# Performance work log

Measured on AMD Instinct MI355X. Metric: run time of the kernel, lower is better.

The kernel has to match this reference:

```python
import jax, jax.numpy as jnp
import numpy as np

N, H, W = 4, 96, 96
C, G, K = 128, 8, 3
GC = C // G          # group channels = 16
P = K * K            # sampling points per group = 9
PAD = K // 2
OFS = 1.0            # offset_scale
HID = 4 * C          # mlp hidden
EPS = 1e-5           # torch nn.LayerNorm default eps


def _ln(x, g, b):
    m = jnp.mean(x, -1, keepdims=True)
    v = jnp.mean((x - m) ** 2, -1, keepdims=True)
    return (x - m) * jax.lax.rsqrt(v + EPS) * g + b


def _dcnv3_core(x, offset, mask):
    # x: (n,H,W,C) channels-last, offset: (n,H,W,G*P*2), mask: (n,H,W,G,P) softmaxed.
    # Faithful port of dcnv3_core_pytorch (stride=1, dilation=1, zero-pad grid_sample,
    # align_corners=False -> pixel = loc*size - 0.5).
    n = x.shape[0]
    xp = jnp.pad(x, ((0, 0), (PAD, PAD), (PAD, PAD), (0, 0)))
    Hin, Win = H + 2 * PAD, W + 2 * PAD
    L = H * W
    base = (K - 1) // 2 + 0.5
    ref_x = (base + jnp.arange(W, dtype=x.dtype)) / Win  # normalized by padded size
    ref_y = (base + jnp.arange(H, dtype=x.dtype)) / Hin
    k = jnp.arange(K, dtype=x.dtype) - (K - 1) // 2
    dx = jnp.repeat(k, K) / Win  # torch meshgrid('ij'): kernel-x varies slowest
    dy = jnp.tile(k, K) / Hin
    off = offset.reshape(n, H, W, G, P, 2)
    # absolute sampling pixel coords (grid_sample align_corners=False)
    px = (ref_x[None, None, :, None, None] + dx * OFS + off[..., 0] * OFS / Win) * Win - 0.5
    py = (ref_y[None, :, None, None, None] + dy * OFS + off[..., 1] * OFS / Hin) * Hin - 0.5
    # layout (n,G,L,P)
    px = px.transpose(0, 3, 1, 2, 4).reshape(n, G, L, P)
    py = py.transpose(0, 3, 1, 2, 4).reshape(n, G, L, P)
    mk = mask.transpose(0, 3, 1, 2, 4).reshape(n, G, L, P)
    xg = xp.reshape(n, Hin * Win, G, GC).transpose(0, 2, 1, 3)
    x0 = jnp.floor(px); y0 = jnp.floor(py)
    fx = px - x0; fy = py - y0
    x0 = x0.astype(jnp.int32); y0 = y0.astype(jnp.int32)
    x1 = x0 + 1; y1 = y0 + 1
    out = jnp.zeros((n, G, L, GC), x.dtype)
    for yi, xi, w in ((y0, x0, (1 - fy) * (1 - fx)), (y0, x1, (1 - fy) * fx),
                      (y1, x0, fy * (1 - fx)), (y1, x1, fy * fx)):
        valid = (yi >= 0) & (yi < Hin) & (xi >= 0) & (xi < Win)
        idx = jnp.clip(yi, 0, Hin - 1) * Win + jnp.clip(xi, 0, Win - 1)
        v = jnp.take_along_axis(xg, idx.reshape(n, G, L * P, 1), axis=2)
        v = v.reshape(n, G, L, P, GC)
        out = out + jnp.einsum('nglp,nglpc->nglc', jnp.where(valid, w, 0.0) * mk, v)
    return out.transpose(0, 2, 1, 3).reshape(n, H, W, C)


def _dcn(x, w_in, b_in, dw_k, dw_b, dwg, dwb, w_off, b_off, w_msk, b_msk, w_out, b_out):
    n = x.shape[0]
    xproj = x @ w_in + b_in
    x1 = jax.lax.conv_general_dilated(
        x, dw_k, (1, 1), 'SAME',
        dimension_numbers=('NHWC', 'HWIO', 'NHWC'),
        feature_group_count=C) + dw_b
    x1 = jax.nn.gelu(_ln(x1, dwg, dwb), approximate=False)
    offset = x1 @ w_off + b_off
    mask = jax.nn.softmax((x1 @ w_msk + b_msk).reshape(n, H, W, G, P), axis=-1)
    y = _dcnv3_core(xproj, offset, mask)
    return y @ w_out + b_out


def setup_inputs() -> dict:
    key = jax.random.key(0)
    ks = jax.random.split(key, 10)
    rn = lambda k, s, sc: jax.random.normal(k, s, jnp.float32) * sc
    return {
        'x': rn(ks[0], (N, H, W, C), 1.0),
        'ln1g': jnp.ones((C,), jnp.float32), 'ln1b': jnp.zeros((C,), jnp.float32),
        'w_in': rn(ks[1], (C, C), 0.02), 'b_in': jnp.zeros((C,), jnp.float32),
        'dw_k': rn(ks[2], (K, K, 1, C), 0.1), 'dw_b': jnp.zeros((C,), jnp.float32),
        'dwg': jnp.ones((C,), jnp.float32), 'dwb': jnp.zeros((C,), jnp.float32),
        'w_off': rn(ks[3], (C, G * P * 2), 0.01), 'b_off': rn(ks[4], (G * P * 2,), 0.1),
        'w_msk': rn(ks[5], (C, G * P), 0.02), 'b_msk': jnp.zeros((G * P,), jnp.float32),
        'w_out': rn(ks[6], (C, C), 0.02), 'b_out': jnp.zeros((C,), jnp.float32),
        'ln2g': jnp.ones((C,), jnp.float32), 'ln2b': jnp.zeros((C,), jnp.float32),
        'w1': rn(ks[7], (C, HID), 0.02), 'b1': jnp.zeros((HID,), jnp.float32),
        'w2': rn(ks[8], (HID, C), 0.02), 'b2': jnp.zeros((C,), jnp.float32),
    }


def reference(x, ln1g, ln1b, w_in, b_in, dw_k, dw_b, dwg, dwb, w_off, b_off,
              w_msk, b_msk, w_out, b_out, ln2g, ln2b, w1, b1, w2, b2):
    # pre-norm InternImage block: x = x + dcn(LN1(x)); x = x + mlp(LN2(x))
    x = x + _dcn(_ln(x, ln1g, ln1b), w_in, b_in, dw_k, dw_b, dwg, dwb,
                 w_off, b_off, w_msk, b_msk, w_out, b_out)
    h = _ln(x, ln2g, ln2b)
    h = jax.nn.gelu(h @ w1 + b1, approximate=False) @ w2 + b2
    return x + h
```

## Files before the change

### kernel.cpp

```cpp
#include <hip/hip_runtime.h>
#include <hip/hip_bf16.h>
#include <math.h>

using bf16 = __hip_bfloat16;
using bf162 = __hip_bfloat162;

typedef __bf16 bf16x8 __attribute__((ext_vector_type(8)));
typedef float floatx4 __attribute__((ext_vector_type(4)));

constexpr int NB = 4, HH = 96, WW = 96, CC = 128, GG = 8, PP = 9;
constexpr int HW = HH * WW;
constexpr int NPIX = NB * HW;

__device__ __forceinline__ float ld1(const float* p) { return *p; }
__device__ __forceinline__ float ld1(const bf16* p)  { return __bfloat162float(*p); }
__device__ __forceinline__ void st1(float* p, float v) { *p = v; }
__device__ __forceinline__ void st1(bf16* p, float v)  { *p = __float2bfloat16(v); }
__device__ __forceinline__ float b2f(bf16 v) { return __bfloat162float(v); }
__device__ __forceinline__ bf16 f2b(float v) { return __float2bfloat16(v); }
__device__ __forceinline__ float gelu_exact(float v) {
    return 0.5f * v * (1.0f + erff(v * 0.7071067811865475f));
}
__device__ __forceinline__ floatx4 MFMA(bf16x8 a, bf16x8 b, floatx4 c) {
    return __builtin_amdgcn_mfma_f32_16x16x32_bf16(a, b, c, 0, 0, 0);
}

struct PrepArgs {
    const float* src[6];
    bf16* dst[6];
    int K[6], N[6];
    int cum[7];
    const float* b_off; const float* b_msk; float* b_om;
};

__global__ __launch_bounds__(256) void prep_weights(PrepArgs pa, int total)
{
    int t = blockIdx.x * 256 + threadIdx.x;
    if (t >= total) return;
    if (t >= pa.cum[6]) {
        int e = t - pa.cum[6];
        pa.b_om[e] = (e < 144) ? pa.b_off[e] : pa.b_msk[e - 144];
        return;
    }
    int i = 0;
    #pragma unroll
    for (int j = 0; j < 5; ++j) if (t >= pa.cum[j + 1]) i = j + 1;
    int e = t - pa.cum[i];
    int Ki = pa.K[i], Ni = pa.N[i];
    int n = e / Ki, k = e - n * Ki;
    pa.dst[i][e] = f2b(pa.src[i][(size_t)k * Ni + n]);
}

template<typename TI, typename TO>
__global__ __launch_bounds__(256) void ln_kernel(
    const TI* __restrict__ X, const float* __restrict__ g,
    const float* __restrict__ b, TO* __restrict__ out)
{
    int wave = (blockIdx.x * 256 + threadIdx.x) >> 6;
    int lane = threadIdx.x & 63;
    if (wave >= NPIX) return;
    const TI* xp = X + (size_t)wave * 128 + 2 * lane;
    float v0 = ld1(xp), v1 = ld1(xp + 1);
    float s = v0 + v1, q = v0 * v0 + v1 * v1;
    #pragma unroll
    for (int o = 32; o; o >>= 1) { s += __shfl_xor(s, o); q += __shfl_xor(q, o); }
    float mean = s * (1.0f / 128.0f);
    float rstd = rsqrtf(q * (1.0f / 128.0f) - mean * mean + 1e-5f);
    float g0 = g[2 * lane], g1 = g[2 * lane + 1];
    float b0 = b[2 * lane], b1 = b[2 * lane + 1];
    TO* op = out + (size_t)wave * 128 + 2 * lane;
    st1(op,     (v0 - mean) * rstd * g0 + b0);
    st1(op + 1, (v1 - mean) * rstd * g1 + b1);
}

__global__ __launch_bounds__(256) void dwconv_ln_gelu_kernel(
    const bf16* __restrict__ xln, const float* __restrict__ dwk,
    const float* __restrict__ dwb, const float* __restrict__ gam,
    const float* __restrict__ bet, bf16* __restrict__ out)
{
    int wave = (blockIdx.x * 256 + threadIdx.x) >> 6;
    int lane = threadIdx.x & 63;
    if (wave >= NPIX) return;
    int n = wave / HW; int rem = wave % HW;
    int y = rem / WW;  int x = rem % WW;
    const bf162* xp = (const bf162*)xln;
    float a0 = 0.f, a1 = 0.f;
    #pragma unroll
    for (int ky = 0; ky < 3; ++ky) {
        int yy = y + ky - 1;
        if (yy < 0 || yy >= HH) continue;
        #pragma unroll
        for (int kx = 0; kx < 3; ++kx) {
            int xx = x + kx - 1;
            if (xx < 0 || xx >= WW) continue;
            bf162 v = xp[((size_t)(n * HH + yy) * WW + xx) * 64 + lane];
            const float* w = dwk + (ky * 3 + kx) * CC + 2 * lane;
            a0 = fmaf(b2f(v.x), w[0], a0);
            a1 = fmaf(b2f(v.y), w[1], a1);
        }
    }
    a0 += dwb[2 * lane]; a1 += dwb[2 * lane + 1];
    float s = a0 + a1, q = a0 * a0 + a1 * a1;
    #pragma unroll
    for (int o = 32; o; o >>= 1) { s += __shfl_xor(s, o); q += __shfl_xor(q, o); }
    float mean = s * (1.0f / 128.0f);
    float rstd = rsqrtf(q * (1.0f / 128.0f) - mean * mean + 1e-5f);
    float h0 = gelu_exact((a0 - mean) * rstd * gam[2 * lane]     + bet[2 * lane]);
    float h1 = gelu_exact((a1 - mean) * rstd * gam[2 * lane + 1] + bet[2 * lane + 1]);
    bf162 o2; o2.x = f2b(h0); o2.y = f2b(h1);
    ((bf162*)out)[(size_t)wave * 64 + lane] = o2;
}

__global__ __launch_bounds__(256) void gemm_mfma_kernel(
    const bf16* __restrict__ A, const bf16* __restrict__ Wt,
    const float* __restrict__ bias, bf16* __restrict__ Out, int M, int Nn)
{
    __shared__ __align__(16) __bf16 As[64][136];
    __shared__ __align__(16) __bf16 Bs[64][136];
    int tid = threadIdx.x;
    int wv = tid >> 6, lane = tid & 63;
    int bm = blockIdx.y * 64, bn = blockIdx.x * 64;
    int mI = lane & 15, q = lane >> 4;

    #pragma unroll
    for (int i = 0; i < 4; ++i) {
        int s = tid + 256 * i;
        int row = s >> 4, ko = (s & 15) * 8;
        *reinterpret_cast<uint4*>(&As[row][ko]) =
            *reinterpret_cast<const uint4*>(A + (size_t)(bm + row) * 128 + ko);
        int ng = bn + row;
        uint4 bv = make_uint4(0, 0, 0, 0);
        if (ng < Nn) bv = *reinterpret_cast<const uint4*>(Wt + (size_t)ng * 128 + ko);
        *reinterpret_cast<uint4*>(&Bs[row][ko]) = bv;
    }
    __syncthreads();

    floatx4 acc[4] = {};
    #pragma unroll
    for (int ks = 0; ks < 4; ++ks) {
        int k = ks * 32 + q * 8;
        bf16x8 a = *reinterpret_cast<const bf16x8*>(&As[wv * 16 + mI][k]);
        #pragma unroll
        for (int t = 0; t < 4; ++t) {
            bf16x8 b = *reinterpret_cast<const bf16x8*>(&Bs[t * 16 + mI][k]);
            acc[t] = MFMA(a, b, acc[t]);
        }
    }
    int row0 = bm + wv * 16 + q * 4;
    #pragma unroll
    for (int t = 0; t < 4; ++t) {
        int col = bn + t * 16 + mI;
        if (col >= Nn) continue;
        float bs = bias[col];
        #pragma unroll
        for (int r = 0; r < 4; ++r)
            st1(Out + (size_t)(row0 + r) * Nn + col, acc[t][r] + bs);
    }
}

constexpr int SOMR = 228;
__global__ __launch_bounds__(256) void dcn_fused_kernel(
    const bf16* __restrict__ xproj, const bf16* __restrict__ x1,
    const bf16* __restrict__ w_omT, const float* __restrict__ b_om,
    bf16* __restrict__ out)
{
    __shared__ __align__(16) __bf16 sX1[16][136];
    __shared__ __align__(16) __bf16 sOmr[16][SOMR];
    __shared__ int4   sOff[4][72];
    __shared__ float4 sW[4][72];
    int tid = threadIdx.x, wv = tid >> 6, lane = tid & 63;
    int mI = lane & 15, q = lane >> 4;
    int bp = blockIdx.x * 16;

    {
        int row = tid >> 4, ko = (tid & 15) * 8;
        *reinterpret_cast<uint4*>(&sX1[row][ko]) =
            *reinterpret_cast<const uint4*>(x1 + (size_t)(bp + row) * 128 + ko);
    }
    __syncthreads();

    {
        bf16x8 a[4];
        #pragma unroll
        for (int ks = 0; ks < 4; ++ks)
            a[ks] = *reinterpret_cast<const bf16x8*>(&sX1[mI][ks * 32 + q * 8]);
        for (int t = wv; t < 14; t += 4) {
            int ng = t * 16 + mI;
            floatx4 acc = {};
            #pragma unroll
            for (int ks = 0; ks < 4; ++ks) {
                bf16x8 b = {};
                if (ng < 216)
                    b = *reinterpret_cast<const bf16x8*>(
                        w_omT + (size_t)ng * 128 + ks * 32 + q * 8);
                acc = MFMA(a[ks], b, acc);
            }
            float bs = (ng < 216) ? b_om[ng] : 0.f;
            #pragma unroll
            for (int r = 0; r < 4; ++r)
                sOmr[q * 4 + r][ng] = *(__bf16*)&(const bf16&)f2b(acc[r] + bs);
        }
    }
    __syncthreads();

    for (int pp = 0; pp < 4; ++pp) {
        int pr = wv * 4 + pp;
        int pix = bp + pr;
        int n = pix / HW; int rem = pix % HW;
        int iy = rem / WW; int ix = rem % WW;

        for (int e = lane; e < 72; e += 64) {
            int g = e / 9, p = e - 9 * g;
            float mx = -1e30f;
            #pragma unroll
            for (int i = 0; i < 9; ++i)
                mx = fmaxf(mx, b2f(*(const bf16*)&sOmr[pr][144 + g * 9 + i]));
            float ssum = 0.f;
            #pragma unroll
            for (int i = 0; i < 9; ++i)
                ssum += __expf(b2f(*(const bf16*)&sOmr[pr][144 + g * 9 + i]) - mx);
            float mw = __expf(b2f(*(const bf16*)&sOmr[pr][144 + e]) - mx) / ssum;

            float ox = b2f(*(const bf16*)&sOmr[pr][g * 18 + 2 * p]);
            float oy = b2f(*(const bf16*)&sOmr[pr][g * 18 + 2 * p + 1]);
            int kx = p / 3 - 1, ky = p % 3 - 1;
            float px = (float)(ix + kx) + ox;
            float py = (float)(iy + ky) + oy;
            float fx0 = floorf(px), fy0 = floorf(py);
            int x0 = (int)fx0, y0 = (int)fy0;
            float fx = px - fx0, fy = py - fy0;
            bool vx0 = (x0 >= 0) & (x0 < WW), vx1 = (x0 + 1 >= 0) & (x0 + 1 < WW);
            bool vy0 = (y0 >= 0) & (y0 < HH), vy1 = (y0 + 1 >= 0) & (y0 + 1 < HH);
            float w00 = (1.f - fy) * (1.f - fx) * mw * (vy0 && vx0 ? 1.f : 0.f);
            float w01 = (1.f - fy) * fx         * mw * (vy0 && vx1 ? 1.f : 0.f);
            float w10 = fy * (1.f - fx)         * mw * (vy1 && vx0 ? 1.f : 0.f);
            float w11 = fy * fx                 * mw * (vy1 && vx1 ? 1.f : 0.f);
            int x0c = min(max(x0, 0), WW - 1), x1c = min(max(x0 + 1, 0), WW - 1);
            int y0c = min(max(y0, 0), HH - 1), y1c = min(max(y0 + 1, 0), HH - 1);
            sOff[wv][e] = make_int4((y0c * WW + x0c) * CC, (y0c * WW + x1c) * CC,
                                    (y1c * WW + x0c) * CC, (y1c * WW + x1c) * CC);
            sW[wv][e] = make_float4(w00, w01, w10, w11);
        }

        const bf16* xb = xproj + (size_t)n * HW * CC + 2 * lane;
        int gbase = (lane >> 3) * 9;
        float a0 = 0.f, a1 = 0.f;
        #pragma unroll
        for (int p = 0; p < 9; ++p) {
            int4 o = sOff[wv][gbase + p];
            float4 w = sW[wv][gbase + p];
            bf162 v00 = *(const bf162*)(xb + o.x);
            bf162 v01 = *(const bf162*)(xb + o.y);
            bf162 v10 = *(const bf162*)(xb + o.z);
            bf162 v11 = *(const bf162*)(xb + o.w);
            a0 += w.x * b2f(v00.x) + w.y * b2f(v01.x) + w.z * b2f(v10.x) + w.w * b2f(v11.x);
            a1 += w.x * b2f(v00.y) + w.y * b2f(v01.y) + w.z * b2f(v10.y) + w.w * b2f(v11.y);
        }
        bf162 o2; o2.x = f2b(a0); o2.y = f2b(a1);
        ((bf162*)out)[(size_t)pix * 64 + lane] = o2;
    }
}

__global__ __launch_bounds__(256, 3) void fused_tail_kernel(
    const bf16* __restrict__ ycore, const float* __restrict__ x,
    const bf16* __restrict__ w_outT, const float* __restrict__ b_out,
    const float* __restrict__ ln2g, const float* __restrict__ ln2b,
    const bf16* __restrict__ w1T, const float* __restrict__ b1,
    const bf16* __restrict__ w2T, const float* __restrict__ b2,
    float* __restrict__ out)
{
    __shared__ __align__(16) bf16 sA[64 * 136];
    __shared__ __align__(16) bf16 sXres[64 * 136];
    __shared__ __align__(16) bf16 sH2[64 * 136];
    int tid = threadIdx.x, wv = tid >> 6, lane = tid & 63;
    int mI = lane & 15, q = lane >> 4;
    int bm = blockIdx.x * 64;

    bf16x8 bw0[4][2];
    #pragma unroll
    for (int ks = 0; ks < 4; ++ks)
        #pragma unroll
        for (int ct = 0; ct < 2; ++ct)
            bw0[ks][ct] = *reinterpret_cast<const bf16x8*>(
                w_outT + (size_t)(wv * 32 + ct * 16 + mI) * 128 + ks * 32 + q * 8);

    #pragma unroll
    for (int i = 0; i < 4; ++i) {
        int s = tid + 256 * i;
        int row = s >> 4, ko = (s & 15) * 8;
        *reinterpret_cast<uint4*>(&sA[row * 136 + ko]) =
            *reinterpret_cast<const uint4*>(ycore + (size_t)(bm + row) * 128 + ko);
    }
    __syncthreads();

    floatx4 acc0[4][2] = {};
    #pragma unroll
    for (int ks = 0; ks < 4; ++ks) {
        int k = ks * 32 + q * 8;
        bf16x8 a[4];
        #pragma unroll
        for (int rt = 0; rt < 4; ++rt)
            a[rt] = *reinterpret_cast<const bf16x8*>(&sA[(rt * 16 + mI) * 136 + k]);
        #pragma unroll
        for (int ct = 0; ct < 2; ++ct)
            #pragma unroll
            for (int rt = 0; rt < 4; ++rt)
                acc0[rt][ct] = MFMA(a[rt], bw0[ks][ct], acc0[rt][ct]);
    }
    #pragma unroll
    for (int rt = 0; rt < 4; ++rt)
        #pragma unroll
        for (int ct = 0; ct < 2; ++ct) {
            int col = wv * 32 + ct * 16 + mI;
            float bs = b_out[col];
            #pragma unroll
            for (int r = 0; r < 4; ++r) {
                int row = rt * 16 + q * 4 + r;
                float v = acc0[rt][ct][r] + bs + x[(size_t)(bm + row) * 128 + col];
                sXres[row * 136 + col] = f2b(v);
            }
        }
    __syncthreads();

    {
        int row = tid >> 2, part = tid & 3;
        float s = 0.f, sq = 0.f;
        float vals[32];
        #pragma unroll
        for (int j = 0; j < 4; ++j) {
            bf16x8 v = *reinterpret_cast<const bf16x8*>(&sXres[row * 136 + part * 32 + j * 8]);
            #pragma unroll
            for (int e = 0; e < 8; ++e) {
                float f = (float)v[e];
                vals[j * 8 + e] = f; s += f; sq += f * f;
            }
        }
        s  += __shfl_xor(s, 1);  s += __shfl_xor(s, 2);
        sq += __shfl_xor(sq, 1); sq += __shfl_xor(sq, 2);
        float mean = s * (1.0f / 128.0f);
        float rstd = rsqrtf(sq * (1.0f / 128.0f) - mean * mean + 1e-5f);
        #pragma unroll
        for (int j = 0; j < 4; ++j) {
            bf16x8 o;
            #pragma unroll
            for (int e = 0; e < 8; ++e) {
                int ch = part * 32 + j * 8 + e;
                bf16 t = f2b((vals[j * 8 + e] - mean) * rstd * ln2g[ch] + ln2b[ch]);
                o[e] = *reinterpret_cast<__bf16*>(&t);
            }
            *reinterpret_cast<bf16x8*>(&sH2[row * 136 + part * 32 + j * 8]) = o;
        }
    }
    __syncthreads();

    floatx4 acc2[4][2] = {};
    #pragma unroll 1
    for (int ph = 0; ph < 4; ++ph) {
        bf16x8 bw1[4][2];
        #pragma unroll
        for (int ks = 0; ks < 4; ++ks)
            #pragma unroll
            for (int ct = 0; ct < 2; ++ct)
                bw1[ks][ct] = *reinterpret_cast<const bf16x8*>(
                    w1T + (size_t)(ph * 128 + wv * 32 + ct * 16 + mI) * 128 + ks * 32 + q * 8);
        floatx4 acc1[4][2] = {};
        #pragma unroll
        for (int ks = 0; ks < 4; ++ks) {
            int k = ks * 32 + q * 8;
            bf16x8 a[4];
            #pragma unroll
            for (int rt = 0; rt < 4; ++rt)
                a[rt] = *reinterpret_cast<const bf16x8*>(&sH2[(rt * 16 + mI) * 136 + k]);
            #pragma unroll
            for (int ct = 0; ct < 2; ++ct)
                #pragma unroll
                for (int rt = 0; rt < 4; ++rt)
                    acc1[rt][ct] = MFMA(a[rt], bw1[ks][ct], acc1[rt][ct]);
        }
        __syncthreads();
        bf16x8 bw2[4][2];
        #pragma unroll
        for (int ks = 0; ks < 4; ++ks)
            #pragma unroll
            for (int ct = 0; ct < 2; ++ct)
                bw2[ks][ct] = *reinterpret_cast<const bf16x8*>(
                    w2T + (size_t)(wv * 32 + ct * 16 + mI) * 512 + ph * 128 + ks * 32 + q * 8);
        #pragma unroll
        for (int rt = 0; rt < 4; ++rt)
            #pragma unroll
            for (int ct = 0; ct < 2; ++ct) {
                int lcol = wv * 32 + ct * 16 + mI;
                float bs = b1[ph * 128 + lcol];
                #pragma unroll
                for (int r = 0; r < 4; ++r) {
                    int row = rt * 16 + q * 4 + r;
                    sA[row * 136 + lcol] = f2b(gelu_exact(acc1[rt][ct][r] + bs));
                }
            }
        __syncthreads();
        #pragma unroll
        for (int ks = 0; ks < 4; ++ks) {
            int k = ks * 32 + q * 8;
            bf16x8 a[4];
            #pragma unroll
            for (int rt = 0; rt < 4; ++rt)
                a[rt] = *reinterpret_cast<const bf16x8*>(&sA[(rt * 16 + mI) * 136 + k]);
            #pragma unroll
            for (int ct = 0; ct < 2; ++ct)
                #pragma unroll
                for (int rt = 0; rt < 4; ++rt)
                    acc2[rt][ct] = MFMA(a[rt], bw2[ks][ct], acc2[rt][ct]);
        }
    }
    #pragma unroll
    for (int rt = 0; rt < 4; ++rt)
        #pragma unroll
        for (int ct = 0; ct < 2; ++ct) {
            int col = wv * 32 + ct * 16 + mI;
            float bs = b2[col];
            #pragma unroll
            for (int r = 0; r < 4; ++r) {
                int row = rt * 16 + q * 4 + r;
                out[(size_t)(bm + row) * 128 + col] =
                    acc2[rt][ct][r] + bs + b2f(sXres[row * 136 + col]);
            }
        }
}

extern "C" void kernel_launch(void* const* d_in, const int* in_sizes, int n_in,
                              void* d_out, int out_size, void* d_ws, size_t ws_size,
                              hipStream_t stream)
{
    const float* x     = (const float*)d_in[0];
    const float* ln1g  = (const float*)d_in[1];
    const float* ln1b  = (const float*)d_in[2];
    const float* w_in  = (const float*)d_in[3];
    const float* b_in  = (const float*)d_in[4];
    const float* dw_k  = (const float*)d_in[5];
    const float* dw_b  = (const float*)d_in[6];
    const float* dwg   = (const float*)d_in[7];
    const float* dwb   = (const float*)d_in[8];
    const float* w_off = (const float*)d_in[9];
    const float* b_off = (const float*)d_in[10];
    const float* w_msk = (const float*)d_in[11];
    const float* b_msk = (const float*)d_in[12];
    const float* w_out = (const float*)d_in[13];
    const float* b_out = (const float*)d_in[14];
    const float* ln2g  = (const float*)d_in[15];
    const float* ln2b  = (const float*)d_in[16];
    const float* w1    = (const float*)d_in[17];
    const float* b1    = (const float*)d_in[18];
    const float* w2    = (const float*)d_in[19];
    const float* b2    = (const float*)d_in[20];
    float* out = (float*)d_out;

    bf16* ws = (bf16*)d_ws;
    bf16* xln   = ws;
    bf16* xproj = xln   + (size_t)NPIX * 128;
    bf16* x1    = xproj + (size_t)NPIX * 128;
    bf16* ycore = xln;
    bf16* wT    = ws + (size_t)NPIX * 600;
    bf16* w_inT  = wT;
    bf16* w_omT  = w_inT  + 16384;
    bf16* w_outT = w_omT  + 27648;
    bf16* w1T    = w_outT + 16384;
    bf16* w2T    = w1T    + 65536;
    float* b_om  = (float*)(w2T + 65536);
    const int WTOT = 191488 + 216;

    PrepArgs pa;
    pa.src[0] = w_in;  pa.dst[0] = w_inT;            pa.K[0] = 128; pa.N[0] = 128;
    pa.src[1] = w_off; pa.dst[1] = w_omT;            pa.K[1] = 128; pa.N[1] = 144;
    pa.src[2] = w_msk; pa.dst[2] = w_omT + 144*128;  pa.K[2] = 128; pa.N[2] = 72;
    pa.src[3] = w_out; pa.dst[3] = w_outT;           pa.K[3] = 128; pa.N[3] = 128;
    pa.src[4] = w1;    pa.dst[4] = w1T;              pa.K[4] = 128; pa.N[4] = 512;
    pa.src[5] = w2;    pa.dst[5] = w2T;              pa.K[5] = 512; pa.N[5] = 128;
    pa.cum[0] = 0;     pa.cum[1] = 16384;  pa.cum[2] = 34816; pa.cum[3] = 44032;
    pa.cum[4] = 60416; pa.cum[5] = 125952; pa.cum[6] = 191488;
    pa.b_off = b_off;  pa.b_msk = b_msk;   pa.b_om = b_om;

    const int M = NPIX;
    dim3 blk(256);

    prep_weights<<<(WTOT + 255) / 256, blk, 0, stream>>>(pa, WTOT);
    ln_kernel<float, bf16><<<NPIX / 4, blk, 0, stream>>>(x, ln1g, ln1b, xln);
    gemm_mfma_kernel<<<dim3(2, M / 64), blk, 0, stream>>>(
        xln, w_inT, b_in, xproj, M, 128);
    dwconv_ln_gelu_kernel<<<NPIX / 4, blk, 0, stream>>>(xln, dw_k, dw_b, dwg, dwb, x1);
    dcn_fused_kernel<<<NPIX / 16, blk, 0, stream>>>(xproj, x1, w_omT, b_om, ycore);
    fused_tail_kernel<<<M / 64, blk, 0, stream>>>(
        ycore, x, w_outT, b_out, ln2g, ln2b, w1T, b1, w2T, b2, out);
}
```

Baseline: 235.4 us.

## Process two pixels per wave with 4-channel vector gathers in DCN sampling

The DCN sampling loop now handles two pixels per wave iteration, with each lane gathering 4 bf16 channels (8 bytes) per corner instead of 2. The softmax max and sum are computed once per group by 16 lanes and shared through LDS, rather than being recomputed for every sampling point. Pixel coordinates come from the block base, on the assumption that a 16-pixel block never crosses an image row since 96 is a multiple of 16. The aim is fewer, wider gather loads, better lane utilisation in the weight-setup phase, and less redundant exp work, at the cost of extra shared memory.

```diff
diff --git a/kernel.cpp b/kernel.cpp
--- a/kernel.cpp
+++ b/kernel.cpp
@@ -166,8 +166,9 @@
 {
     __shared__ __align__(16) __bf16 sX1[16][136];
     __shared__ __align__(16) __bf16 sOmr[16][SOMR];
-    __shared__ int4   sOff[4][72];
-    __shared__ float4 sW[4][72];
+    __shared__ int4   sOff[4][2][72];
+    __shared__ float4 sW[4][2][72];
+    __shared__ float  sStat[4][16][2];
     int tid = threadIdx.x, wv = tid >> 6, lane = tid & 63;
     int mI = lane & 15, q = lane >> 4;
     int bp = blockIdx.x * 16;
@@ -203,14 +204,16 @@
     }
     __syncthreads();
 
-    for (int pp = 0; pp < 4; ++pp) {
-        int pr = wv * 4 + pp;
-        int pix = bp + pr;
-        int n = pix / HW; int rem = pix % HW;
-        int iy = rem / WW; int ix = rem % WW;
-
-        for (int e = lane; e < 72; e += 64) {
-            int g = e / 9, p = e - 9 * g;
+    int n   = bp / HW;
+    int rem0 = bp % HW;
+    int iy  = rem0 / WW;
+    int ix0 = rem0 % WW;
+
+    for (int half = 0; half < 2; ++half) {
+        int prBase = wv * 4 + half * 2;
+        if (lane < 16) {
+            int pr = prBase + (lane >> 3);
+            int g = lane & 7;
             float mx = -1e30f;
             #pragma unroll
             for (int i = 0; i < 9; ++i)
@@ -219,12 +222,21 @@
             #pragma unroll
             for (int i = 0; i < 9; ++i)
                 ssum += __expf(b2f(*(const bf16*)&sOmr[pr][144 + g * 9 + i]) - mx);
-            float mw = __expf(b2f(*(const bf16*)&sOmr[pr][144 + e]) - mx) / ssum;
+            sStat[wv][lane][0] = mx;
+            sStat[wv][lane][1] = ssum;
+        }
+        for (int e = lane; e < 144; e += 64) {
+            int pixL = e / 72, ee = e - pixL * 72;
+            int g = ee / 9, p = ee - 9 * g;
+            int pr = prBase + pixL;
+            float mx  = sStat[wv][pixL * 8 + g][0];
+            float ssum = sStat[wv][pixL * 8 + g][1];
+            float mw = __expf(b2f(*(const bf16*)&sOmr[pr][144 + ee]) - mx) / ssum;
 
             float ox = b2f(*(const bf16*)&sOmr[pr][g * 18 + 2 * p]);
             float oy = b2f(*(const bf16*)&sOmr[pr][g * 18 + 2 * p + 1]);
             int kx = p / 3 - 1, ky = p % 3 - 1;
-            float px = (float)(ix + kx) + ox;
+            float px = (float)(ix0 + pr + kx) + ox;
             float py = (float)(iy + ky) + oy;
             float fx0 = floorf(px), fy0 = floorf(py);
             int x0 = (int)fx0, y0 = (int)fy0;
@@ -237,27 +249,44 @@
             float w11 = fy * fx                 * mw * (vy1 && vx1 ? 1.f : 0.f);
             int x0c = min(max(x0, 0), WW - 1), x1c = min(max(x0 + 1, 0), WW - 1);
             int y0c = min(max(y0, 0), HH - 1), y1c = min(max(y0 + 1, 0), HH - 1);
-            sOff[wv][e] = make_int4((y0c * WW + x0c) * CC, (y0c * WW + x1c) * CC,
-                                    (y1c * WW + x0c) * CC, (y1c * WW + x1c) * CC);
-            sW[wv][e] = make_float4(w00, w01, w10, w11);
-        }
-
-        const bf16* xb = xproj + (size_t)n * HW * CC + 2 * lane;
-        int gbase = (lane >> 3) * 9;
-        float a0 = 0.f, a1 = 0.f;
-        #pragma unroll
-        for (int p = 0; p < 9; ++p) {
-            int4 o = sOff[wv][gbase + p];
-            float4 w = sW[wv][gbase + p];
-            bf162 v00 = *(const bf162*)(xb + o.x);
-            bf162 v01 = *(const bf162*)(xb + o.y);
-            bf162 v10 = *(const bf162*)(xb + o.z);
-            bf162 v11 = *(const bf162*)(xb + o.w);
-            a0 += w.x * b2f(v00.x) + w.y * b2f(v01.x) + w.z * b2f(v10.x) + w.w * b2f(v11.x);
-            a1 += w.x * b2f(v00.y) + w.y * b2f(v01.y) + w.z * b2f(v10.y) + w.w * b2f(v11.y);
-        }
-        bf162 o2; o2.x = f2b(a0); o2.y = f2b(a1);
-        ((bf162*)out)[(size_t)pix * 64 + lane] = o2;
+            sOff[wv][pixL][ee] = make_int4(
+                (y0c * WW + x0c) * (CC * 2), (y0c * WW + x1c) * (CC * 2),
+                (y1c * WW + x0c) * (CC * 2), (y1c * WW + x1c) * (CC * 2));
+            sW[wv][pixL][ee] = make_float4(w00, w01, w10, w11);
+        }
+        {
+            int pixL = lane >> 5;
+            int g = (lane >> 2) & 7;
+            int c4 = lane & 3;
+            int pr = prBase + pixL;
+            int pix = bp + pr;
+            const char* xb = (const char*)(xproj + (size_t)n * HW * CC
+                                           + g * 16 + c4 * 4);
+            float a0 = 0.f, a1 = 0.f, a2 = 0.f, a3 = 0.f;
+            #pragma unroll
+            for (int p = 0; p < 9; ++p) {
+                int4 o = sOff[wv][pixL][g * 9 + p];
+                float4 w = sW[wv][pixL][g * 9 + p];
+                ushort4 v00 = *(const ushort4*)(xb + o.x);
+                ushort4 v01 = *(const ushort4*)(xb + o.y);
+                ushort4 v10 = *(const ushort4*)(xb + o.z);
+                ushort4 v11 = *(const ushort4*)(xb + o.w);
+                a0 += w.x * b2f(*(const bf16*)&v00.x) + w.y * b2f(*(const bf16*)&v01.x)
+                    + w.z * b2f(*(const bf16*)&v10.x) + w.w * b2f(*(const bf16*)&v11.x);
+                a1 += w.x * b2f(*(const bf16*)&v00.y) + w.y * b2f(*(const bf16*)&v01.y)
+                    + w.z * b2f(*(const bf16*)&v10.y) + w.w * b2f(*(const bf16*)&v11.y);
+                a2 += w.x * b2f(*(const bf16*)&v00.z) + w.y * b2f(*(const bf16*)&v01.z)
+                    + w.z * b2f(*(const bf16*)&v10.z) + w.w * b2f(*(const bf16*)&v11.z);
+                a3 += w.x * b2f(*(const bf16*)&v00.w) + w.y * b2f(*(const bf16*)&v01.w)
+                    + w.z * b2f(*(const bf16*)&v10.w) + w.w * b2f(*(const bf16*)&v11.w);
+            }
+            ushort4 ov;
+            bf16 t0 = f2b(a0); ov.x = *(unsigned short*)&t0;
+            bf16 t1 = f2b(a1); ov.y = *(unsigned short*)&t1;
+            bf16 t2 = f2b(a2); ov.z = *(unsigned short*)&t2;
+            bf16 t3 = f2b(a3); ov.w = *(unsigned short*)&t3;
+            *(ushort4*)(out + (size_t)pix * 128 + g * 16 + c4 * 4) = ov;
+        }
     }
 }
 
```

New measurement: 235.6 us. Within noise of the previous version (+0.1%).
